# Kernel optimization log

Measured on AMD Instinct MI355X. Metric: run time of the kernel, lower is better.

Reference implementation:

```python
import jax, jax.numpy as jnp
import numpy as np

H, D, G = 8, 64, 64          # num_heads, head_dim, num_slices
HID = H * D                  # 512
EPS = 1e-5
N = 100000


def setup_inputs() -> dict:
    key = jax.random.key(0)
    ks = jax.random.split(key, 16)
    s = 0.02  # init scale
    return {
        "x": jax.random.normal(ks[0], (N, HID), dtype=jnp.float32),
        # x_proj / fx_proj: Linear(HID -> HID) with bias, eqx stores W as (out, in)
        "Wx": jax.random.normal(ks[1], (HID, HID), dtype=jnp.float32) * s,
        "bx": jax.random.normal(ks[2], (HID,), dtype=jnp.float32) * s,
        "Wfx": jax.random.normal(ks[3], (HID, HID), dtype=jnp.float32) * s,
        "bfx": jax.random.normal(ks[4], (HID,), dtype=jnp.float32) * s,
        # slice_proj: Linear(D -> G) with bias
        "Ws": jax.random.normal(ks[5], (G, D), dtype=jnp.float32) * s,
        "bs": jax.random.normal(ks[6], (G,), dtype=jnp.float32) * s,
        # learned temperature, init 0.5, shape (H,1,1)
        "temperature": jnp.ones((H, 1, 1), dtype=jnp.float32) * 0.5,
        # slice MultiheadAttention (num_heads=1, size D): q/k/v/out proj, no biases (eqx defaults)
        "Wq": jax.random.normal(ks[7], (D, D), dtype=jnp.float32) * s,
        "Wk": jax.random.normal(ks[8], (D, D), dtype=jnp.float32) * s,
        "Wv": jax.random.normal(ks[9], (D, D), dtype=jnp.float32) * s,
        "Wo": jax.random.normal(ks[10], (D, D), dtype=jnp.float32) * s,
        # out_proj: Linear(HID -> HID) with bias
        "Wout": jax.random.normal(ks[11], (HID, HID), dtype=jnp.float32) * s,
        "bout": jax.random.normal(ks[12], (HID,), dtype=jnp.float32) * s,
    }


def reference(x, Wx, bx, Wfx, bfx, Ws, bs, temperature, Wq, Wk, Wv, Wo, Wout, bout):
    n = x.shape[0]
    # token projections, split into heads: (H, N, D)
    x_mid = (x @ Wx.T + bx).reshape(n, H, D).transpose(1, 0, 2)
    fx_mid = (x @ Wfx.T + bfx).reshape(n, H, D).transpose(1, 0, 2)

    # slice weights: proj -> temperature-scaled softmax over G  (H, N, G)
    logits = jnp.einsum('hnd,gd->hng', x_mid, Ws) + bs
    w = jax.nn.softmax(logits * temperature, axis=-1)

    # weighted pooling to slice tokens (H, G, D)
    norm = w.sum(axis=1)                                   # (H, G)
    tokens = jnp.einsum('hnd,hng->hgd', fx_mid, w) / (norm[..., None] + EPS)

    # small single-head attention over the G slice tokens, vmapped over H
    q = jnp.einsum('hgd,od->hgo', tokens, Wq)
    k = jnp.einsum('hgd,od->hgo', tokens, Wk)
    v = jnp.einsum('hgd,od->hgo', tokens, Wv)
    attn = jax.nn.softmax(jnp.einsum('hgd,hkd->hgk', q, k) / jnp.sqrt(jnp.float32(D)), axis=-1)
    out_tok = jnp.einsum('hgk,hkd->hgd', attn, v)
    out_tok = jnp.einsum('hgd,od->hgo', out_tok, Wo)

    # deslice: weighted unpooling back to tokens, merge heads, output projection
    out = jnp.einsum('hgd,hng->hnd', out_tok, w)           # (H, N, D)
    out = out.transpose(1, 0, 2).reshape(n, HID)
    return out @ Wout.T + bout
```

## Files before the change

### kernel.cpp

```cpp
#include <hip/hip_runtime.h>
#include <hip/hip_bf16.h>

#define HID 512
#define NH  8
#define DD  64
#define GG  64
#define EPSF 1e-5f

typedef __attribute__((ext_vector_type(8))) short short8;
typedef __attribute__((ext_vector_type(4))) float floatx4;

__device__ __forceinline__ short f2bf(float f) {
    union { float f; unsigned u; } v; v.f = f;
    unsigned r = v.u + 0x7fffu + ((v.u >> 16) & 1u);
    return (short)(r >> 16);
}

#define GLOAD_LDS16(g, l) __builtin_amdgcn_global_load_lds( \
    (const __attribute__((address_space(1))) unsigned int*)(g), \
    (__attribute__((address_space(3))) unsigned int*)(l), 16, 0, 0)

__global__ void fold1_kernel(const float* __restrict__ Wx, const float* __restrict__ bx,
                             const float* __restrict__ Wfx, const float* __restrict__ bfx,
                             const float* __restrict__ Ws, const float* __restrict__ bs,
                             const float* __restrict__ temp,
                             short* __restrict__ Wcat, float* __restrict__ bias_cat) {
    int idx = blockIdx.x * 256 + threadIdx.x;
    int row = idx >> 9;
    int k = idx & 511;
    float val;
    if (row < 512) {
        val = Wfx[row * 512 + k];
        if (k == 0) bias_cat[row] = bfx[row];
    } else {
        int hg = row - 512;
        int h = hg >> 6, g = hg & 63;
        float t = temp[h];
        float s = 0.f;
        #pragma unroll 8
        for (int d = 0; d < 64; ++d) s += Ws[g * 64 + d] * Wx[(h * 64 + d) * 512 + k];
        val = s * t;
        if (k == 0) {
            float b = 0.f;
            for (int d = 0; d < 64; ++d) b += Ws[g * 64 + d] * bx[h * 64 + d];
            bias_cat[row] = (b + bs[g]) * t;
        }
    }
    Wcat[idx] = f2bf(val);
}

__global__ __launch_bounds__(256, 4)
void gemm1_fused(const float* __restrict__ X,
                 const short* __restrict__ B,
                 const float* __restrict__ bias,
                 short* __restrict__ Cp,
                 int M, int clog2, int Rtiles) {
    const int K = 512, lda = 512, ldc = 1024;
    __shared__ short As[128 * 64];
    __shared__ short Bs[128 * 64];

    const int id = blockIdx.x;
    const int xcd = id & 7;
    const int s = id >> 3;
    const int cblk = s & ((1 << clog2) - 1);
    const int slice = (Rtiles + 7) >> 3;
    const int rt = xcd * slice + (s >> clog2);
    if (rt >= Rtiles) return;

    const int tid = threadIdx.x;
    const int wid = tid >> 6, lane = tid & 63;
    const int col0 = cblk * 128;
    const int row0 = rt * 128;
    const int wm = (wid >> 1) * 64, wn = (wid & 1) * 64;
    const int lr = lane & 15, lq = lane >> 4;

    int st_row[4], st_kc[4];
    const float* aptr[4];
    #pragma unroll
    for (int it = 0; it < 4; ++it) {
        int c = tid + it * 256;
        st_row[it] = c >> 3;
        st_kc[it] = (c & 7) ^ (st_row[it] & 7);
        int ar = min(row0 + st_row[it], M - 1);
        aptr[it] = X + (size_t)ar * lda + st_kc[it] * 8;
    }
    const int fx0 = (lq ^ (lr & 7)) * 8;
    const int fx1 = ((4 + lq) ^ (lr & 7)) * 8;

    floatx4 acc[4][4];
    #pragma unroll
    for (int i = 0; i < 4; ++i)
        #pragma unroll
        for (int j = 0; j < 4; ++j) acc[i][j] = (floatx4)(0.f);

    const short* Bbase = B + (size_t)col0 * lda;

    float4 fa[4][2];
    #pragma unroll
    for (int it = 0; it < 4; ++it) {
        fa[it][0] = *(const float4*)(aptr[it]);
        fa[it][1] = *(const float4*)(aptr[it] + 4);
    }

    for (int k0 = 0; k0 < K; k0 += 64) {
        #pragma unroll
        for (int it = 0; it < 4; ++it) {
            short* ldsB = Bs + (wid * 64 + it * 256) * 8;
            GLOAD_LDS16(Bbase + (size_t)st_row[it] * lda + k0 + st_kc[it] * 8, ldsB);
        }
        #pragma unroll
        for (int it = 0; it < 4; ++it) {
            short8 sv;
            sv[0] = f2bf(fa[it][0].x); sv[1] = f2bf(fa[it][0].y);
            sv[2] = f2bf(fa[it][0].z); sv[3] = f2bf(fa[it][0].w);
            sv[4] = f2bf(fa[it][1].x); sv[5] = f2bf(fa[it][1].y);
            sv[6] = f2bf(fa[it][1].z); sv[7] = f2bf(fa[it][1].w);
            *(short8*)&As[(size_t)(tid + it * 256) * 8] = sv;
        }
        __syncthreads();

        const int kn = (k0 + 64 < K) ? (k0 + 64) : 0;
        #pragma unroll
        for (int it = 0; it < 4; ++it) {
            fa[it][0] = *(const float4*)(aptr[it] + kn);
            fa[it][1] = *(const float4*)(aptr[it] + kn + 4);
        }

        short8 af[4], bfr[4];
        #pragma unroll
        for (int i = 0; i < 4; ++i) af[i]  = *(const short8*)&As[(wm + i * 16 + lr) * 64 + fx0];
        #pragma unroll
        for (int j = 0; j < 4; ++j) bfr[j] = *(const short8*)&Bs[(wn + j * 16 + lr) * 64 + fx0];
        #pragma unroll
        for (int i = 0; i < 4; ++i)
            #pragma unroll
            for (int j = 0; j < 4; ++j)
                acc[i][j] = __builtin_amdgcn_mfma_f32_16x16x32_bf16(af[i], bfr[j], acc[i][j], 0, 0, 0);
        #pragma unroll
        for (int i = 0; i < 4; ++i) af[i]  = *(const short8*)&As[(wm + i * 16 + lr) * 64 + fx1];
        #pragma unroll
        for (int j = 0; j < 4; ++j) bfr[j] = *(const short8*)&Bs[(wn + j * 16 + lr) * 64 + fx1];
        #pragma unroll
        for (int i = 0; i < 4; ++i)
            #pragma unroll
            for (int j = 0; j < 4; ++j)
                acc[i][j] = __builtin_amdgcn_mfma_f32_16x16x32_bf16(af[i], bfr[j], acc[i][j], 0, 0, 0);
        __syncthreads();
    }

    const bool do_sm = (col0 >= 512);
    float bcol[4];
    #pragma unroll
    for (int j = 0; j < 4; ++j) bcol[j] = bias[col0 + wn + j * 16 + lr];

    #pragma unroll
    for (int i = 0; i < 4; ++i) {
        #pragma unroll
        for (int r = 0; r < 4; ++r) {
            int grow = row0 + wm + i * 16 + lq * 4 + r;
            float v[4];
            #pragma unroll
            for (int j = 0; j < 4; ++j) v[j] = acc[i][j][r] + bcol[j];
            if (do_sm) {
                float m = fmaxf(fmaxf(v[0], v[1]), fmaxf(v[2], v[3]));
                #pragma unroll
                for (int off = 1; off < 16; off <<= 1) m = fmaxf(m, __shfl_xor(m, off));
                float sum = 0.f;
                #pragma unroll
                for (int j = 0; j < 4; ++j) { v[j] = __expf(v[j] - m); sum += v[j]; }
                #pragma unroll
                for (int off = 1; off < 16; off <<= 1) sum += __shfl_xor(sum, off);
                float inv = 1.f / sum;
                #pragma unroll
                for (int j = 0; j < 4; ++j) v[j] *= inv;
            }
            if (grow < M) {
                #pragma unroll
                for (int j = 0; j < 4; ++j) {
                    int gcol = col0 + wn + j * 16 + lr;
                    Cp[(size_t)grow * ldc + gcol] = f2bf(v[j]);
                }
            }
        }
    }
}

template <bool OUT_F32, bool FUSE_SM>
__global__ __launch_bounds__(256, 4)
void gemm_bt(const short* __restrict__ A, int lda,
             const short* __restrict__ B,
             const float* __restrict__ bias,
             void* __restrict__ Cp, int ldc,
             int M, int K, int clog2, int Rtiles) {
    __shared__ short As[128 * 64];
    __shared__ short Bs[128 * 64];

    const int id = blockIdx.x;
    const int xcd = id & 7;
    const int s = id >> 3;
    const int cblk = s & ((1 << clog2) - 1);
    const int slice = (Rtiles + 7) >> 3;
    const int rt = xcd * slice + (s >> clog2);
    if (rt >= Rtiles) return;

    const int tid = threadIdx.x;
    const int wid = tid >> 6, lane = tid & 63;
    const int col0 = cblk * 128;
    const int row0 = rt * 128;
    const int wm = (wid >> 1) * 64, wn = (wid & 1) * 64;
    const int lr = lane & 15, lq = lane >> 4;

    int st_row[4], st_kc[4];
    #pragma unroll
    for (int it = 0; it < 4; ++it) {
        int c = tid + it * 256;
        st_row[it] = c >> 3;
        st_kc[it] = (c & 7) ^ (st_row[it] & 7);
    }
    const int fx0 = (lq ^ (lr & 7)) * 8;
    const int fx1 = ((4 + lq) ^ (lr & 7)) * 8;

    floatx4 acc[4][4];
    #pragma unroll
    for (int i = 0; i < 4; ++i)
        #pragma unroll
        for (int j = 0; j < 4; ++j) acc[i][j] = (floatx4)(0.f);

    const short* Abase = A + (size_t)row0 * lda;
    const short* Bbase = B + (size_t)col0 * lda;

    for (int k0 = 0; k0 < K; k0 += 64) {
        #pragma unroll
        for (int it = 0; it < 4; ++it) {
            short* ldsA = As + (wid * 64 + it * 256) * 8;
            short* ldsB = Bs + (wid * 64 + it * 256) * 8;
            GLOAD_LDS16(Abase + (size_t)st_row[it] * lda + k0 + st_kc[it] * 8, ldsA);
            GLOAD_LDS16(Bbase + (size_t)st_row[it] * lda + k0 + st_kc[it] * 8, ldsB);
        }
        __syncthreads();

        short8 af[4], bfr[4];
        #pragma unroll
        for (int i = 0; i < 4; ++i) af[i]  = *(const short8*)&As[(wm + i * 16 + lr) * 64 + fx0];
        #pragma unroll
        for (int j = 0; j < 4; ++j) bfr[j] = *(const short8*)&Bs[(wn + j * 16 + lr) * 64 + fx0];
        #pragma unroll
        for (int i = 0; i < 4; ++i)
            #pragma unroll
            for (int j = 0; j < 4; ++j)
                acc[i][j] = __builtin_amdgcn_mfma_f32_16x16x32_bf16(af[i], bfr[j], acc[i][j], 0, 0, 0);
        #pragma unroll
        for (int i = 0; i < 4; ++i) af[i]  = *(const short8*)&As[(wm + i * 16 + lr) * 64 + fx1];
        #pragma unroll
        for (int j = 0; j < 4; ++j) bfr[j] = *(const short8*)&Bs[(wn + j * 16 + lr) * 64 + fx1];
        #pragma unroll
        for (int i = 0; i < 4; ++i)
            #pragma unroll
            for (int j = 0; j < 4; ++j)
                acc[i][j] = __builtin_amdgcn_mfma_f32_16x16x32_bf16(af[i], bfr[j], acc[i][j], 0, 0, 0);
        __syncthreads();
    }

    const bool do_sm = FUSE_SM && (col0 >= 512);
    float bcol[4];
    #pragma unroll
    for (int j = 0; j < 4; ++j) bcol[j] = bias[col0 + wn + j * 16 + lr];

    #pragma unroll
    for (int i = 0; i < 4; ++i) {
        #pragma unroll
        for (int r = 0; r < 4; ++r) {
            int grow = row0 + wm + i * 16 + lq * 4 + r;
            float v[4];
            #pragma unroll
            for (int j = 0; j < 4; ++j) v[j] = acc[i][j][r] + bcol[j];
            if (do_sm) {
                float m = fmaxf(fmaxf(v[0], v[1]), fmaxf(v[2], v[3]));
                #pragma unroll
                for (int off = 1; off < 16; off <<= 1) m = fmaxf(m, __shfl_xor(m, off));
                float sum = 0.f;
                #pragma unroll
                for (int j = 0; j < 4; ++j) { v[j] = __expf(v[j] - m); sum += v[j]; }
                #pragma unroll
                for (int off = 1; off < 16; off <<= 1) sum += __shfl_xor(sum, off);
                float inv = 1.f / sum;
                #pragma unroll
                for (int j = 0; j < 4; ++j) v[j] *= inv;
            }
            if (grow < M) {
                #pragma unroll
                for (int j = 0; j < 4; ++j) {
                    int gcol = col0 + wn + j * 16 + lr;
                    if constexpr (OUT_F32) ((float*)Cp)[(size_t)grow * ldc + gcol] = v[j];
                    else                   ((short*)Cp)[(size_t)grow * ldc + gcol] = f2bf(v[j]);
                }
            }
        }
    }
}

__global__ __launch_bounds__(256)
void pool_mfma(const short* __restrict__ mid, float* __restrict__ tok_raw,
               float* __restrict__ norm, int N, int chunk) {
    const int h = blockIdx.y;
    const int n0 = blockIdx.x * chunk;
    if (n0 >= N) return;
    const int ksteps = (min(chunk, N - n0)) >> 5;

    const int tid = threadIdx.x;
    const int wid = tid >> 6, lane = tid & 63;
    const int lr = lane & 15, lq = lane >> 4;
    const int wg = (wid >> 1) * 32, wd = (wid & 1) * 32;

    __shared__ short wt[32 * 72];
    __shared__ short ft[32 * 72];

    const int sn = tid >> 3;
    const int sc0 = (tid & 7) * 8;
    const int scr = (sc0 + 16 * ((sn >> 3) & 3)) & 63;
    const int st_off = sn * 72 + scr;

    const int ra = ((wg + lr) + 16 * lq) & 63;
    const int rb = ((wd + lr) + 16 * lq) & 63;

    const short* wbase = mid + (size_t)n0 * 1024 + 512 + h * 64;
    const short* fbase = mid + (size_t)n0 * 1024 + h * 64;

    floatx4 acc[2][2];
    #pragma unroll
    for (int i = 0; i < 2; ++i)
        #pragma unroll
        for (int j = 0; j < 2; ++j) acc[i][j] = (floatx4)(0.f);
    floatx4 accn[2];
    accn[0] = (floatx4)(0.f); accn[1] = (floatx4)(0.f);

    short8 ones;
    #pragma unroll
    for (int j = 0; j < 8; ++j) ones[j] = (short)0x3F80;

    for (int ks = 0; ks < ksteps; ++ks) {
        const size_t roff = (size_t)(ks * 32 + sn) * 1024;
        short8 wv = *(const short8*)(wbase + roff + sc0);
        short8 fv = *(const short8*)(fbase + roff + sc0);
        __syncthreads();
        *(short8*)&wt[st_off] = wv;
        *(short8*)&ft[st_off] = fv;
        __syncthreads();

        short8 af[2], bf_[2];
        #pragma unroll
        for (int i = 0; i < 2; ++i) {
            short tmpv[8];
            #pragma unroll
            for (int j = 0; j < 8; ++j)
                tmpv[j] = wt[(lq * 8 + j) * 72 + ((ra + i * 16) & 63)];
            af[i] = *(const short8*)tmpv;
        }
        #pragma unroll
        for (int j2 = 0; j2 < 2; ++j2) {
            short tmpv[8];
            #pragma unroll
            for (int j = 0; j < 8; ++j)
                tmpv[j] = ft[(lq * 8 + j) * 72 + ((rb + j2 * 16) & 63)];
            bf_[j2] = *(const short8*)tmpv;
        }
        #pragma unroll
        for (int i = 0; i < 2; ++i)
            #pragma unroll
            for (int j = 0; j < 2; ++j)
                acc[i][j] = __builtin_amdgcn_mfma_f32_16x16x32_bf16(af[i], bf_[j], acc[i][j], 0, 0, 0);
        if (wd == 0) {
            #pragma unroll
            for (int i = 0; i < 2; ++i)
                accn[i] = __builtin_amdgcn_mfma_f32_16x16x32_bf16(af[i], ones, accn[i], 0, 0, 0);
        }
    }

    #pragma unroll
    for (int i = 0; i < 2; ++i) {
        #pragma unroll
        for (int r = 0; r < 4; ++r) {
            int g = wg + i * 16 + lq * 4 + r;
            #pragma unroll
            for (int j = 0; j < 2; ++j) {
                int d = wd + j * 16 + lr;
                atomicAdd(&tok_raw[(h * 64 + g) * 64 + d], acc[i][j][r]);
            }
        }
    }
    if (wd == 0 && lr == 0) {
        #pragma unroll
        for (int i = 0; i < 2; ++i)
            #pragma unroll
            for (int r = 0; r < 4; ++r)
                atomicAdd(&norm[h * 64 + wg + i * 16 + lq * 4 + r], accn[i][r]);
    }
}

__global__ __launch_bounds__(256)
void attn_kernel(const float* __restrict__ tok_raw, const float* __restrict__ norm,
                 const float* __restrict__ Wq, const float* __restrict__ Wk,
                 const float* __restrict__ Wv, const float* __restrict__ Wo,
                 float* __restrict__ out_tok) {
    const int h = blockIdx.x;
    const int tid = threadIdx.x;
    const int g = tid & 63, part = tid >> 6;
    const int o0 = part * 16;

    __shared__ float tk[64][65];
    __shared__ float qq[64][65];
    __shared__ float kk[64][65];
    __shared__ float vv[64][65];
    __shared__ float pp[64][65];
    __shared__ float od[64][65];

    const float inv = 1.f / (norm[h * 64 + g] + EPSF);
    #pragma unroll
    for (int dd = 0; dd < 16; ++dd) {
        int d = o0 + dd;
        tk[g][d] = tok_raw[(size_t)(h * 64 + g) * 64 + d] * inv;
    }
    __syncthreads();

    float t[64];
    #pragma unroll
    for (int d = 0; d < 64; ++d) t[d] = tk[g][d];
    #pragma unroll
    for (int oo = 0; oo < 16; ++oo) {
        int o = o0 + oo;
        float sq = 0.f, sk = 0.f, sv = 0.f;
        #pragma unroll
        for (int d = 0; d < 64; ++d) {
            float td = t[d];
            sq += td * Wq[o * 64 + d];
            sk += td * Wk[o * 64 + d];
            sv += td * Wv[o * 64 + d];
        }
        qq[g][o] = sq; kk[g][o] = sk; vv[g][o] = sv;
    }
    __syncthreads();

    float q[64];
    #pragma unroll
    for (int o = 0; o < 64; ++o) q[o] = qq[g][o];
    #pragma unroll
    for (int jj = 0; jj < 16; ++jj) {
        int j = o0 + jj;
        float s = 0.f;
        #pragma unroll
        for (int o = 0; o < 64; ++o) s += q[o] * kk[j][o];
        pp[g][j] = s * 0.125f;
    }
    __syncthreads();

    float sr[64];
    float mx = -1e30f;
    #pragma unroll
    for (int j = 0; j < 64; ++j) { sr[j] = pp[g][j]; mx = fmaxf(mx, sr[j]); }
    float sum = 0.f;
    #pragma unroll
    for (int j = 0; j < 64; ++j) { sr[j] = __expf(sr[j] - mx); sum += sr[j]; }
    const float isum = 1.f / sum;

    #pragma unroll
    for (int dd = 0; dd < 16; ++dd) {
        int d = o0 + dd;
        float a = 0.f;
        #pragma unroll
        for (int j = 0; j < 64; ++j) a += sr[j] * vv[j][d];
        od[g][d] = a * isum;
    }
    __syncthreads();

    float ot[64];
    #pragma unroll
    for (int d = 0; d < 64; ++d) ot[d] = od[g][d];
    #pragma unroll
    for (int oo = 0; oo < 16; ++oo) {
        int o = o0 + oo;
        float a = 0.f;
        #pragma unroll
        for (int d = 0; d < 64; ++d) a += ot[d] * Wo[o * 64 + d];
        out_tok[(size_t)(h * 64 + g) * 64 + o] = a;
    }
}

__global__ void fold2_kernel(const float* __restrict__ out_tok,
                             const float* __restrict__ Wout, short* __restrict__ Vbf) {
    int idx = blockIdx.x * 256 + threadIdx.x;
    int o = idx >> 9, hg = idx & 511;
    int h = hg >> 6;
    const float* ot = out_tok + (size_t)hg * 64;
    const float* wo = Wout + (size_t)o * 512 + h * 64;
    float s = 0.f;
    #pragma unroll 8
    for (int d = 0; d < 64; ++d) s += ot[d] * wo[d];
    Vbf[idx] = f2bf(s);
}

extern "C" void kernel_launch(void* const* d_in, const int* in_sizes, int n_in,
                              void* d_out, int out_size, void* d_ws, size_t ws_size,
                              hipStream_t stream) {
    const float* x    = (const float*)d_in[0];
    const float* Wx   = (const float*)d_in[1];
    const float* bx   = (const float*)d_in[2];
    const float* Wfx  = (const float*)d_in[3];
    const float* bfx  = (const float*)d_in[4];
    const float* Ws   = (const float*)d_in[5];
    const float* bs   = (const float*)d_in[6];
    const float* temp = (const float*)d_in[7];
    const float* Wq   = (const float*)d_in[8];
    const float* Wk   = (const float*)d_in[9];
    const float* Wv   = (const float*)d_in[10];
    const float* Wo   = (const float*)d_in[11];
    const float* Wout = (const float*)d_in[12];
    const float* bout = (const float*)d_in[13];

    const int N = in_sizes[0] / HID;

    char* p = (char*)d_ws;
    short* mid = (short*)p;           p += (size_t)N * 1024 * 2;
    short* Wcat = (short*)p;          p += (size_t)1024 * 512 * 2;
    float* bias_cat = (float*)p;      p += 1024 * 4;
    float* tok_raw = (float*)p;       p += (size_t)NH * GG * DD * 4;
    float* norm_ = (float*)p;         p += (size_t)NH * GG * 4;
    float* out_tok = (float*)p;       p += (size_t)NH * GG * DD * 4;
    short* Vbf = (short*)p;           p += (size_t)512 * 512 * 2;

    fold1_kernel<<<2048, 256, 0, stream>>>(Wx, bx, Wfx, bfx, Ws, bs, temp, Wcat, bias_cat);
    hipMemsetAsync(tok_raw, 0, (size_t)(NH * GG * DD + NH * GG) * 4, stream);

    const int R = (N + 127) / 128;
    const int slice = (R + 7) / 8;

    gemm1_fused<<<8 * slice * 8, 256, 0, stream>>>(
        x, Wcat, bias_cat, mid, N, 3, R);

    const int chunk = 544;
    dim3 g2((N + chunk - 1) / chunk, 8);
    pool_mfma<<<g2, 256, 0, stream>>>(mid, tok_raw, norm_, N, chunk);

    attn_kernel<<<8, 256, 0, stream>>>(tok_raw, norm_, Wq, Wk, Wv, Wo, out_tok);

    fold2_kernel<<<1024, 256, 0, stream>>>(out_tok, Wout, Vbf);

    gemm_bt<true, false><<<8 * slice * 4, 256, 0, stream>>>(
        mid + 512, 1024, Vbf, bout, d_out, HID, N, 512, 2, R);
}
```

Before: 738.5 us.

## Fuse slice pooling into first projection GEMM and drop fx intermediate

The first GEMM now runs 512-thread blocks that each compute a 128-row tile covering both the fx columns and the matching slice-weight columns for two heads. The pooling reduction (w^T·fx and the slice norms) then happens in-block through LDS with MFMA and atomics, which replaces the separate pool kernel. Only the softmaxed slice weights are written to global memory (N×512 bf16 instead of N×1024), cutting writes and the pool kernel's re-read. In exchange there are more atomics per row tile, higher LDS use and register pressure, and occupancy drops to two blocks per CU.

```diff
diff --git a/kernel.cpp b/kernel.cpp
--- a/kernel.cpp
+++ b/kernel.cpp
@@ -8,6 +8,7 @@
 #define EPSF 1e-5f
 
 typedef __attribute__((ext_vector_type(8))) short short8;
+typedef __attribute__((ext_vector_type(4))) short short4v;
 typedef __attribute__((ext_vector_type(4))) float floatx4;
 
 __device__ __forceinline__ short f2bf(float f) {
@@ -49,41 +50,46 @@
     Wcat[idx] = f2bf(val);
 }
 
-__global__ __launch_bounds__(256, 4)
-void gemm1_fused(const float* __restrict__ X,
-                 const short* __restrict__ B,
-                 const float* __restrict__ bias,
-                 short* __restrict__ Cp,
-                 int M, int clog2, int Rtiles) {
-    const int K = 512, lda = 512, ldc = 1024;
-    __shared__ short As[128 * 64];
-    __shared__ short Bs[128 * 64];
+__global__ __launch_bounds__(512, 2)
+void gemm1_pool(const float* __restrict__ X,
+                const short* __restrict__ Wc,
+                const float* __restrict__ bias,
+                short* __restrict__ Wb,
+                float* __restrict__ tok_raw,
+                float* __restrict__ norm_,
+                int M, int Rtiles) {
+    const int lda = 512;
+    __shared__ short smem[24576];
+    short* As = smem;
+    short* Bs = smem + 8192;
 
     const int id = blockIdx.x;
     const int xcd = id & 7;
     const int s = id >> 3;
-    const int cblk = s & ((1 << clog2) - 1);
+    const int cblk = s & 3;
     const int slice = (Rtiles + 7) >> 3;
-    const int rt = xcd * slice + (s >> clog2);
+    const int rt = xcd * slice + (s >> 2);
     if (rt >= Rtiles) return;
 
     const int tid = threadIdx.x;
     const int wid = tid >> 6, lane = tid & 63;
-    const int col0 = cblk * 128;
+    const int wm = wid >> 2, wn = wid & 3;
+    const int lr = lane & 15, lq = lane >> 4;
     const int row0 = rt * 128;
-    const int wm = (wid >> 1) * 64, wn = (wid & 1) * 64;
-    const int lr = lane & 15, lq = lane >> 4;
-
-    int st_row[4], st_kc[4];
-    const float* aptr[4];
-    #pragma unroll
-    for (int it = 0; it < 4; ++it) {
-        int c = tid + it * 256;
+
+    int st_row[2], st_kc[2];
+    const float* aptr[2];
+    #pragma unroll
+    for (int it = 0; it < 2; ++it) {
+        int c = tid + it * 512;
         st_row[it] = c >> 3;
         st_kc[it] = (c & 7) ^ (st_row[it] & 7);
         int ar = min(row0 + st_row[it], M - 1);
         aptr[it] = X + (size_t)ar * lda + st_kc[it] * 8;
     }
+    const short* Bb0 = Wc + (size_t)(cblk * 128) * lda;
+    const short* Bb1 = Wc + (size_t)(512 + cblk * 128) * lda;
+
     const int fx0 = (lq ^ (lr & 7)) * 8;
     const int fx1 = ((4 + lq) ^ (lr & 7)) * 8;
 
@@ -93,53 +99,54 @@
         #pragma unroll
         for (int j = 0; j < 4; ++j) acc[i][j] = (floatx4)(0.f);
 
-    const short* Bbase = B + (size_t)col0 * lda;
-
-    float4 fa[4][2];
-    #pragma unroll
-    for (int it = 0; it < 4; ++it) {
+    float4 fa[2][2];
+    #pragma unroll
+    for (int it = 0; it < 2; ++it) {
         fa[it][0] = *(const float4*)(aptr[it]);
         fa[it][1] = *(const float4*)(aptr[it] + 4);
     }
 
-    for (int k0 = 0; k0 < K; k0 += 64) {
-        #pragma unroll
-        for (int it = 0; it < 4; ++it) {
-            short* ldsB = Bs + (wid * 64 + it * 256) * 8;
-            GLOAD_LDS16(Bbase + (size_t)st_row[it] * lda + k0 + st_kc[it] * 8, ldsB);
-        }
-        #pragma unroll
-        for (int it = 0; it < 4; ++it) {
+    for (int k0 = 0; k0 < 512; k0 += 64) {
+        #pragma unroll
+        for (int it = 0; it < 2; ++it) {
+            short* d0 = Bs +        (it * 512 + wid * 64) * 8;
+            short* d1 = Bs + 8192 + (it * 512 + wid * 64) * 8;
+            GLOAD_LDS16(Bb0 + (size_t)st_row[it] * lda + k0 + st_kc[it] * 8, d0);
+            GLOAD_LDS16(Bb1 + (size_t)st_row[it] * lda + k0 + st_kc[it] * 8, d1);
+        }
+        #pragma unroll
+        for (int it = 0; it < 2; ++it) {
             short8 sv;
             sv[0] = f2bf(fa[it][0].x); sv[1] = f2bf(fa[it][0].y);
             sv[2] = f2bf(fa[it][0].z); sv[3] = f2bf(fa[it][0].w);
             sv[4] = f2bf(fa[it][1].x); sv[5] = f2bf(fa[it][1].y);
             sv[6] = f2bf(fa[it][1].z); sv[7] = f2bf(fa[it][1].w);
-            *(short8*)&As[(size_t)(tid + it * 256) * 8] = sv;
+            *(short8*)&As[(size_t)(tid + it * 512) * 8] = sv;
         }
         __syncthreads();
 
-        const int kn = (k0 + 64 < K) ? (k0 + 64) : 0;
-        #pragma unroll
-        for (int it = 0; it < 4; ++it) {
+        const int kn = (k0 + 64 < 512) ? (k0 + 64) : 0;
+        #pragma unroll
+        for (int it = 0; it < 2; ++it) {
             fa[it][0] = *(const float4*)(aptr[it] + kn);
             fa[it][1] = *(const float4*)(aptr[it] + kn + 4);
         }
 
+        const int bbase = (wn >> 1) * 8192;
         short8 af[4], bfr[4];
         #pragma unroll
-        for (int i = 0; i < 4; ++i) af[i]  = *(const short8*)&As[(wm + i * 16 + lr) * 64 + fx0];
-        #pragma unroll
-        for (int j = 0; j < 4; ++j) bfr[j] = *(const short8*)&Bs[(wn + j * 16 + lr) * 64 + fx0];
+        for (int i = 0; i < 4; ++i) af[i]  = *(const short8*)&As[(wm * 64 + i * 16 + lr) * 64 + fx0];
+        #pragma unroll
+        for (int j = 0; j < 4; ++j) bfr[j] = *(const short8*)&Bs[bbase + ((wn & 1) * 64 + j * 16 + lr) * 64 + fx0];
         #pragma unroll
         for (int i = 0; i < 4; ++i)
             #pragma unroll
             for (int j = 0; j < 4; ++j)
                 acc[i][j] = __builtin_amdgcn_mfma_f32_16x16x32_bf16(af[i], bfr[j], acc[i][j], 0, 0, 0);
         #pragma unroll
-        for (int i = 0; i < 4; ++i) af[i]  = *(const short8*)&As[(wm + i * 16 + lr) * 64 + fx1];
-        #pragma unroll
-        for (int j = 0; j < 4; ++j) bfr[j] = *(const short8*)&Bs[(wn + j * 16 + lr) * 64 + fx1];
+        for (int i = 0; i < 4; ++i) af[i]  = *(const short8*)&As[(wm * 64 + i * 16 + lr) * 64 + fx1];
+        #pragma unroll
+        for (int j = 0; j < 4; ++j) bfr[j] = *(const short8*)&Bs[bbase + ((wn & 1) * 64 + j * 16 + lr) * 64 + fx1];
         #pragma unroll
         for (int i = 0; i < 4; ++i)
             #pragma unroll
@@ -148,20 +155,20 @@
         __syncthreads();
     }
 
-    const bool do_sm = (col0 >= 512);
     float bcol[4];
-    #pragma unroll
-    for (int j = 0; j < 4; ++j) bcol[j] = bias[col0 + wn + j * 16 + lr];
-
-    #pragma unroll
-    for (int i = 0; i < 4; ++i) {
-        #pragma unroll
-        for (int r = 0; r < 4; ++r) {
-            int grow = row0 + wm + i * 16 + lq * 4 + r;
-            float v[4];
-            #pragma unroll
-            for (int j = 0; j < 4; ++j) v[j] = acc[i][j][r] + bcol[j];
-            if (do_sm) {
+    const int cbase = (wn < 2) ? (cblk * 128 + wn * 64)
+                               : (512 + cblk * 128 + (wn - 2) * 64);
+    #pragma unroll
+    for (int j = 0; j < 4; ++j) bcol[j] = bias[cbase + j * 16 + lr];
+
+    if (wn >= 2) {
+        #pragma unroll
+        for (int i = 0; i < 4; ++i) {
+            #pragma unroll
+            for (int r = 0; r < 4; ++r) {
+                float v[4];
+                #pragma unroll
+                for (int j = 0; j < 4; ++j) v[j] = acc[i][j][r] + bcol[j];
                 float m = fmaxf(fmaxf(v[0], v[1]), fmaxf(v[2], v[3]));
                 #pragma unroll
                 for (int off = 1; off < 16; off <<= 1) m = fmaxf(m, __shfl_xor(m, off));
@@ -170,17 +177,86 @@
                 for (int j = 0; j < 4; ++j) { v[j] = __expf(v[j] - m); sum += v[j]; }
                 #pragma unroll
                 for (int off = 1; off < 16; off <<= 1) sum += __shfl_xor(sum, off);
-                float inv = 1.f / sum;
-                #pragma unroll
-                for (int j = 0; j < 4; ++j) v[j] *= inv;
+                const float inv = 1.f / sum;
+                #pragma unroll
+                for (int j = 0; j < 4; ++j) acc[i][j][r] = v[j] * inv;
             }
-            if (grow < M) {
-                #pragma unroll
-                for (int j = 0; j < 4; ++j) {
-                    int gcol = col0 + wn + j * 16 + lr;
-                    Cp[(size_t)grow * ldc + gcol] = f2bf(v[j]);
+        }
+        #pragma unroll
+        for (int i = 0; i < 4; ++i) {
+            #pragma unroll
+            for (int r = 0; r < 4; ++r) {
+                const int grow = row0 + wm * 64 + i * 16 + lq * 4 + r;
+                if (grow < M) {
+                    #pragma unroll
+                    for (int j = 0; j < 4; ++j)
+                        Wb[(size_t)grow * 512 + cblk * 128 + (wn - 2) * 64 + j * 16 + lr] =
+                            f2bf(acc[i][j][r]);
                 }
             }
+        }
+    } else {
+        #pragma unroll
+        for (int i = 0; i < 4; ++i)
+            #pragma unroll
+            for (int j = 0; j < 4; ++j)
+                #pragma unroll
+                for (int r = 0; r < 4; ++r) acc[i][j][r] += bcol[j];
+    }
+
+    short* wT  = smem;
+    short* fxT = smem + 8704;
+    short8 ones;
+    #pragma unroll
+    for (int j = 0; j < 8; ++j) ones[j] = (short)0x3F80;
+    const int head0 = cblk * 2;
+
+    #pragma unroll 1
+    for (int hp = 0; hp < 2; ++hp) {
+        __syncthreads();
+        if (wn == hp || wn == 2 + hp) {
+            short* dst = (wn >= 2) ? wT : fxT;
+            #pragma unroll
+            for (int i = 0; i < 4; ++i) {
+                #pragma unroll
+                for (int j = 0; j < 4; ++j) {
+                    short4v pk;
+                    #pragma unroll
+                    for (int r = 0; r < 4; ++r) {
+                        const int grow = row0 + wm * 64 + i * 16 + lq * 4 + r;
+                        pk[r] = (grow < M) ? f2bf(acc[i][j][r]) : (short)0;
+                    }
+                    *(short4v*)&dst[(j * 16 + lr) * 136 + wm * 64 + i * 16 + lq * 4] = pk;
+                }
+            }
+        }
+        __syncthreads();
+        const int gi = wid >> 1, djp = wid & 1;
+        floatx4 pacc[2];
+        pacc[0] = (floatx4)(0.f); pacc[1] = (floatx4)(0.f);
+        floatx4 nacc = (floatx4)(0.f);
+        #pragma unroll
+        for (int ks = 0; ks < 4; ++ks) {
+            short8 paf = *(const short8*)&wT[(gi * 16 + lr) * 136 + ks * 32 + lq * 8];
+            #pragma unroll
+            for (int t = 0; t < 2; ++t) {
+                short8 pbf = *(const short8*)&fxT[((djp * 2 + t) * 16 + lr) * 136 + ks * 32 + lq * 8];
+                pacc[t] = __builtin_amdgcn_mfma_f32_16x16x32_bf16(paf, pbf, pacc[t], 0, 0, 0);
+            }
+            if (djp == 0)
+                nacc = __builtin_amdgcn_mfma_f32_16x16x32_bf16(paf, ones, nacc, 0, 0, 0);
+        }
+        const int head = head0 + hp;
+        #pragma unroll
+        for (int t = 0; t < 2; ++t)
+            #pragma unroll
+            for (int r = 0; r < 4; ++r)
+                atomicAdd(&tok_raw[(head * 64 + gi * 16 + lq * 4 + r) * 64 + (djp * 2 + t) * 16 + lr],
+                          pacc[t][r]);
+        if (djp == 0 && lr == 0) {
+            #pragma unroll
+            for (int r = 0; r < 4; ++r)
+                atomicAdd(&norm_[head * 64 + gi * 16 + lq * 4 + r], nacc[r]);
         }
     }
 }
@@ -296,104 +372,6 @@
                 }
             }
         }
-    }
-}
-
-__global__ __launch_bounds__(256)
-void pool_mfma(const short* __restrict__ mid, float* __restrict__ tok_raw,
-               float* __restrict__ norm, int N, int chunk) {
-    const int h = blockIdx.y;
-    const int n0 = blockIdx.x * chunk;
-    if (n0 >= N) return;
-    const int ksteps = (min(chunk, N - n0)) >> 5;
-
-    const int tid = threadIdx.x;
-    const int wid = tid >> 6, lane = tid & 63;
-    const int lr = lane & 15, lq = lane >> 4;
-    const int wg = (wid >> 1) * 32, wd = (wid & 1) * 32;
-
-    __shared__ short wt[32 * 72];
-    __shared__ short ft[32 * 72];
-
-    const int sn = tid >> 3;
-    const int sc0 = (tid & 7) * 8;
-    const int scr = (sc0 + 16 * ((sn >> 3) & 3)) & 63;
-    const int st_off = sn * 72 + scr;
-
-    const int ra = ((wg + lr) + 16 * lq) & 63;
-    const int rb = ((wd + lr) + 16 * lq) & 63;
-
-    const short* wbase = mid + (size_t)n0 * 1024 + 512 + h * 64;
-    const short* fbase = mid + (size_t)n0 * 1024 + h * 64;
-
-    floatx4 acc[2][2];
-    #pragma unroll
-    for (int i = 0; i < 2; ++i)
-        #pragma unroll
-        for (int j = 0; j < 2; ++j) acc[i][j] = (floatx4)(0.f);
-    floatx4 accn[2];
-    accn[0] = (floatx4)(0.f); accn[1] = (floatx4)(0.f);
-
-    short8 ones;
-    #pragma unroll
-    for (int j = 0; j < 8; ++j) ones[j] = (short)0x3F80;
-
-    for (int ks = 0; ks < ksteps; ++ks) {
-        const size_t roff = (size_t)(ks * 32 + sn) * 1024;
-        short8 wv = *(const short8*)(wbase + roff + sc0);
-        short8 fv = *(const short8*)(fbase + roff + sc0);
-        __syncthreads();
-        *(short8*)&wt[st_off] = wv;
-        *(short8*)&ft[st_off] = fv;
-        __syncthreads();
-
-        short8 af[2], bf_[2];
-        #pragma unroll
-        for (int i = 0; i < 2; ++i) {
-            short tmpv[8];
-            #pragma unroll
-            for (int j = 0; j < 8; ++j)
-                tmpv[j] = wt[(lq * 8 + j) * 72 + ((ra + i * 16) & 63)];
-            af[i] = *(const short8*)tmpv;
-        }
-        #pragma unroll
-        for (int j2 = 0; j2 < 2; ++j2) {
-            short tmpv[8];
-            #pragma unroll
-            for (int j = 0; j < 8; ++j)
-                tmpv[j] = ft[(lq * 8 + j) * 72 + ((rb + j2 * 16) & 63)];
-            bf_[j2] = *(const short8*)tmpv;
-        }
-        #pragma unroll
-        for (int i = 0; i < 2; ++i)
-            #pragma unroll
-            for (int j = 0; j < 2; ++j)
-                acc[i][j] = __builtin_amdgcn_mfma_f32_16x16x32_bf16(af[i], bf_[j], acc[i][j], 0, 0, 0);
-        if (wd == 0) {
-            #pragma unroll
-            for (int i = 0; i < 2; ++i)
-                accn[i] = __builtin_amdgcn_mfma_f32_16x16x32_bf16(af[i], ones, accn[i], 0, 0, 0);
-        }
-    }
-
-    #pragma unroll
-    for (int i = 0; i < 2; ++i) {
-        #pragma unroll
-        for (int r = 0; r < 4; ++r) {
-            int g = wg + i * 16 + lq * 4 + r;
-            #pragma unroll
-            for (int j = 0; j < 2; ++j) {
-                int d = wd + j * 16 + lr;
-                atomicAdd(&tok_raw[(h * 64 + g) * 64 + d], acc[i][j][r]);
-            }
-        }
-    }
-    if (wd == 0 && lr == 0) {
-        #pragma unroll
-        for (int i = 0; i < 2; ++i)
-            #pragma unroll
-            for (int r = 0; r < 4; ++r)
-                atomicAdd(&norm[h * 64 + wg + i * 16 + lq * 4 + r], accn[i][r]);
     }
 }
 
@@ -519,7 +497,7 @@
     const int N = in_sizes[0] / HID;
 
     char* p = (char*)d_ws;
-    short* mid = (short*)p;           p += (size_t)N * 1024 * 2;
+    short* w_bf = (short*)p;          p += (size_t)N * 512 * 2;
     short* Wcat = (short*)p;          p += (size_t)1024 * 512 * 2;
     float* bias_cat = (float*)p;      p += 1024 * 4;
     float* tok_raw = (float*)p;       p += (size_t)NH * GG * DD * 4;
@@ -533,17 +511,13 @@
     const int R = (N + 127) / 128;
     const int slice = (R + 7) / 8;
 
-    gemm1_fused<<<8 * slice * 8, 256, 0, stream>>>(
-        x, Wcat, bias_cat, mid, N, 3, R);
-
-    const int chunk = 544;
-    dim3 g2((N + chunk - 1) / chunk, 8);
-    pool_mfma<<<g2, 256, 0, stream>>>(mid, tok_raw, norm_, N, chunk);
+    gemm1_pool<<<8 * slice * 4, 512, 0, stream>>>(
+        x, Wcat, bias_cat, w_bf, tok_raw, norm_, N, R);
 
     attn_kernel<<<8, 256, 0, stream>>>(tok_raw, norm_, Wq, Wk, Wv, Wo, out_tok);
 
     fold2_kernel<<<1024, 256, 0, stream>>>(out_tok, Wout, Vbf);
 
     gemm_bt<true, false><<<8 * slice * 4, 256, 0, stream>>>(
-        mid + 512, 1024, Vbf, bout, d_out, HID, N, 512, 2, R);
-}
+        w_bf, 512, Vbf, bout, d_out, HID, N, 512, 2, R);
+}
```

After: 785.7 us. 6.4% more time.
